# Kernel optimization log

Measured on AMD Instinct MI355X. Metric: run time of the kernel, lower is better.

Reference implementation:

```python
import jax, jax.numpy as jnp
import numpy as np

IS_CAUSAL = True


def setup_inputs() -> dict:
    key = jax.random.key(0)
    kq, kk, kv = jax.random.split(key, 3)
    q = jax.random.normal(kq, (2, 32, 2048, 128), dtype=jnp.float32)
    k = jax.random.normal(kk, (2, 8, 2048, 128), dtype=jnp.float32)
    v = jax.random.normal(kv, (2, 8, 2048, 128), dtype=jnp.float32)
    return {"q": q, "k": k, "v": v}


def reference(q, k, v):
    # q: [B, Hq, Sq, D]; k, v: [B, Hk, Sk, D] with Hq % Hk == 0 (GQA)
    B, Hq, Sq, D = q.shape
    Hk, Sk = k.shape[1], k.shape[2]
    rep = Hq // Hk
    # GQA broadcast: repeat_interleave along head dim
    k_e = jnp.repeat(k, rep, axis=1)  # [B, Hq, Sk, D]
    v_e = jnp.repeat(v, rep, axis=1)
    scale = jnp.float32(1.0 / np.sqrt(D))
    # scores in fp32 (original casts s to float32 before softmax)
    s = jnp.einsum('bhqd,bhkd->bhqk', q, k_e).astype(jnp.float32) * scale
    if IS_CAUSAL:
        mask = jnp.tril(jnp.ones((Sq, Sk), dtype=bool))  # [Sq, Sk]
        s = jnp.where(mask, s, -jnp.inf)
    p = jax.nn.softmax(s, axis=-1).astype(q.dtype)  # [B, Hq, Sq, Sk]
    attn = jnp.einsum('bhqk,bhkd->bhqd', p, v_e)
    return attn
```

## Files before the change

### kernel.cpp

```cpp
#include <hip/hip_runtime.h>


typedef __bf16 bf16_t;
typedef __bf16 bf16x2 __attribute__((ext_vector_type(2)));
typedef __bf16 bf16x8 __attribute__((ext_vector_type(8)));
typedef float f32x4v __attribute__((ext_vector_type(4)));
typedef float f32x16 __attribute__((ext_vector_type(16)));
typedef unsigned int u32;
typedef u32 u32x4 __attribute__((ext_vector_type(4)));

constexpr int B_ = 2, HQ = 32, HK = 8, SQ = 2048, D = 128;
constexpr int QT = 128, KT = 32;
constexpr int NQT = SQ / QT;
constexpr int NT = SQ / KT;
constexpr int NITEM = NQT * 64;
constexpr int NBLK = 768;
constexpr int TILE_ELEM = KT * D * 2;
constexpr size_t TILE_BYTES = TILE_ELEM * 2;
constexpr size_t WS_IMG = (size_t)B_ * HK * NT * TILE_BYTES;
constexpr size_t WS_NEED = WS_IMG + 64;

__device__ __forceinline__ u32 pkbf(float a, float b) {
  bf16x2 t; t[0] = (bf16_t)a; t[1] = (bf16_t)b;
  return __builtin_bit_cast(u32, t);
}
__device__ __forceinline__ float fexp2(float x) { return __builtin_exp2f(x); }

__device__ __forceinline__ void gl_lds16(const void* g, void* l) {
  __builtin_amdgcn_global_load_lds(
      (const __attribute__((address_space(1))) u32*)g,
      (__attribute__((address_space(3))) u32*)l, 16, 0, 0);
}

__global__ __launch_bounds__(256)
void prepass(const float* __restrict__ kg, const float* __restrict__ vg,
             bf16_t* __restrict__ ws) {
  const int blk = blockIdx.x;
  const int bh = blk >> 6, t = blk & 63;
  const float* ksrc = kg + ((size_t)bh * SQ + (size_t)t * KT) * D;
  const float* vsrc = vg + ((size_t)bh * SQ + (size_t)t * KT) * D;
  bf16_t* kdst = ws + (size_t)blk * TILE_ELEM;
  bf16_t* vdst = kdst + KT * D;
  const int tid = threadIdx.x;
#pragma unroll
  for (int i = 0; i < 2; ++i) {
    const int c = tid + 256 * i;
    const int r = c >> 4, p = c & 15, q = p ^ (r & 15);
    const float* s = ksrc + (size_t)r * D + 8 * q;
    f32x4v a = *(const f32x4v*)s;
    f32x4v b = *(const f32x4v*)(s + 4);
    bf16x8 w;
    w[0]=(bf16_t)a[0]; w[1]=(bf16_t)a[1]; w[2]=(bf16_t)a[2]; w[3]=(bf16_t)a[3];
    w[4]=(bf16_t)b[0]; w[5]=(bf16_t)b[1]; w[6]=(bf16_t)b[2]; w[7]=(bf16_t)b[3];
    *(bf16x8*)(kdst + (size_t)r * D + 8 * p) = w;
  }
#pragma unroll
  for (int i = 0; i < 2; ++i) {
    const int c = tid + 256 * i;
    const int d = c >> 2, p = c & 3, q = p ^ (d & 3);
    bf16x8 w;
#pragma unroll
    for (int j = 0; j < 8; ++j) w[j] = (bf16_t)vsrc[(size_t)(8 * q + j) * D + d];
    *(bf16x8*)(vdst + (size_t)d * KT + 8 * p) = w;
  }
}

__global__ __launch_bounds__(256, 3)
void fa6(const float* __restrict__ qg_, const bf16_t* __restrict__ ws,
         float* __restrict__ og_, int* __restrict__ cnt) {
  __shared__ __align__(16) char ldsraw[3 * TILE_BYTES];
  __shared__ int item_s;

  const int tid = threadIdx.x;
  const int wv = tid >> 6, lane = tid & 63;
  const int ln = lane & 31, hx = lane >> 5;
  const float qscale = 0.08838834764831845f * 1.4426950408889634f;

  for (;;) {
    if (tid == 0) item_s = atomicAdd(cnt, 1);
    __syncthreads();
    const int it = item_s;
    if (it >= NITEM) break;

    const int qt = (NQT - 1) - (it >> 6);
    const int bh = it & 63;
    const int b = bh >> 5, h = bh & 31, hk = h >> 2;
    const int q0 = qt * QT;
    const float* qg = qg_ + ((size_t)(b * HQ + h) * SQ + q0) * D;
    float*       og = og_ + ((size_t)(b * HQ + h) * SQ + q0) * D;
    const bf16_t* wsrc = ws + (size_t)(b * HK + hk) * NT * TILE_ELEM;
    const int ntile = q0 / KT + 4;
    const int wrow = q0 + 32 * wv;

    auto stage = [&](int tl, int buf) {
      const char* src = (const char*)(wsrc + (size_t)tl * TILE_ELEM);
      char* dst = ldsraw + (size_t)buf * TILE_BYTES;
#pragma unroll
      for (int i = 0; i < 4; ++i) {
        const int chunk = 4 * wv + i;
        gl_lds16(src + chunk * 1024 + lane * 16, dst + chunk * 1024);
      }
    };

    stage(0, 0);

    bf16x8 qf[8];
    {
      const float* qrp = qg + (size_t)(32 * wv + ln) * D + 8 * hx;
#pragma unroll
      for (int s = 0; s < 8; ++s) {
        f32x4v a = *(const f32x4v*)(qrp + 16 * s);
        f32x4v c = *(const f32x4v*)(qrp + 16 * s + 4);
        bf16x8 t;
        t[0]=(bf16_t)(a[0]*qscale); t[1]=(bf16_t)(a[1]*qscale);
        t[2]=(bf16_t)(a[2]*qscale); t[3]=(bf16_t)(a[3]*qscale);
        t[4]=(bf16_t)(c[0]*qscale); t[5]=(bf16_t)(c[1]*qscale);
        t[6]=(bf16_t)(c[2]*qscale); t[7]=(bf16_t)(c[3]*qscale);
        qf[s] = t;
      }
    }
    stage(1, 1);

    f32x16 Oa[4];
#pragma unroll
    for (int mb = 0; mb < 4; ++mb)
#pragma unroll
      for (int r = 0; r < 16; ++r) Oa[mb][r] = 0.f;
    float m = -1e30f, l = 0.f;

    int cur = 0;
    for (int t = 0; t < ntile; ++t) {
      if (t + 1 < ntile) { asm volatile("s_waitcnt vmcnt(4)" ::: "memory"); }
      else               { asm volatile("s_waitcnt vmcnt(0)" ::: "memory"); }
      __builtin_amdgcn_sched_barrier(0);
      __builtin_amdgcn_s_barrier();
      __builtin_amdgcn_sched_barrier(0);

      if (t + 2 < ntile) {
        const int sb = (cur == 0) ? 2 : cur - 1;
        stage(t + 2, sb);
      }

      const int kb = t * KT;
      if (kb <= wrow) {
        const bf16_t* kbp = (const bf16_t*)(ldsraw + (size_t)cur * TILE_BYTES);
        const bf16_t* vbp = kbp + KT * D;

        f32x16 sa;
#pragma unroll
        for (int r = 0; r < 16; ++r) sa[r] = 0.f;
        __builtin_amdgcn_s_setprio(1);
#pragma unroll
        for (int s = 0; s < 8; ++s) {
          const int cb = (2 * s + hx) ^ (ln & 15);
          bf16x8 kf = *(const bf16x8*)(kbp + ln * 128 + cb * 8);
          sa = __builtin_amdgcn_mfma_f32_32x32x16_bf16(kf, qf[s], sa, 0, 0, 0);
        }
        __builtin_amdgcn_s_setprio(0);

        if (kb == wrow) {
#pragma unroll
          for (int r = 0; r < 16; ++r) {
            const int kl = (r & 3) + 8 * (r >> 2) + 4 * hx;
            if (kl > ln) sa[r] = -1e30f;
          }
        }

        float tm = -1e30f;
#pragma unroll
        for (int r = 0; r < 16; ++r) tm = fmaxf(tm, sa[r]);
        tm = fmaxf(tm, __shfl_xor(tm, 32, 64));
        if (__any(tm > m + 8.f)) {
          const float mn = fmaxf(m, tm);
          const float corr = fexp2(m - mn);
          m = mn; l *= corr;
#pragma unroll
          for (int mb = 0; mb < 4; ++mb)
#pragma unroll
            for (int r = 0; r < 16; ++r) Oa[mb][r] *= corr;
        }
#pragma unroll
        for (int r = 0; r < 16; ++r) sa[r] = fexp2(sa[r] - m);
        float ps = 0.f;
#pragma unroll
        for (int r = 0; r < 16; ++r) ps += sa[r];
        ps += __shfl_xor(ps, 32, 64);
        l += ps;

        u32x4 pa[2];
#pragma unroll
        for (int s2 = 0; s2 < 2; ++s2) {
          const u32 A0 = pkbf(sa[8*s2+0], sa[8*s2+1]);
          const u32 A1 = pkbf(sa[8*s2+2], sa[8*s2+3]);
          const u32 B0 = pkbf(sa[8*s2+4], sa[8*s2+5]);
          const u32 B1 = pkbf(sa[8*s2+6], sa[8*s2+7]);
          const u32 r0 = __shfl_xor(hx ? A0 : B0, 32, 64);
          const u32 r1 = __shfl_xor(hx ? A1 : B1, 32, 64);
          pa[s2][0] = hx ? r0 : A0;
          pa[s2][1] = hx ? r1 : A1;
          pa[s2][2] = hx ? B0 : r0;
          pa[s2][3] = hx ? B1 : r1;
        }

        __builtin_amdgcn_s_setprio(1);
#pragma unroll
        for (int s2 = 0; s2 < 2; ++s2) {
#pragma unroll
          for (int mb = 0; mb < 4; ++mb) {
            const int d0 = ln + 32 * mb;
            const int cb = (2 * s2 + hx) ^ (d0 & 3);
            bf16x8 vf = *(const bf16x8*)(vbp + d0 * KT + cb * 8);
            Oa[mb] = __builtin_amdgcn_mfma_f32_32x32x16_bf16(
                vf, __builtin_bit_cast(bf16x8, pa[s2]), Oa[mb], 0, 0, 0);
          }
        }
        __builtin_amdgcn_s_setprio(0);
      }

      cur = (cur == 2) ? 0 : cur + 1;
    }

    asm volatile("s_waitcnt lgkmcnt(0)" ::: "memory");
    __builtin_amdgcn_s_barrier();
    __builtin_amdgcn_sched_barrier(0);

    const float inv = 1.f / l;
    float* wlds = (float*)ldsraw + wv * 2048;
#pragma unroll
    for (int h2 = 0; h2 < 2; ++h2) {
#pragma unroll
      for (int mb2 = 0; mb2 < 2; ++mb2) {
        const int mb = 2 * h2 + mb2;
#pragma unroll
        for (int g2 = 0; g2 < 4; ++g2) {
          f32x4v v4;
          v4[0] = Oa[mb][4*g2+0] * inv; v4[1] = Oa[mb][4*g2+1] * inv;
          v4[2] = Oa[mb][4*g2+2] * inv; v4[3] = Oa[mb][4*g2+3] * inv;
          const int lslot = 2 * g2 + hx + 8 * mb2;
          const int pslot = lslot ^ (ln & 15);
          *(f32x4v*)(wlds + ln * 64 + pslot * 4) = v4;
        }
      }
      asm volatile("s_waitcnt lgkmcnt(0)" ::: "memory");
      __builtin_amdgcn_sched_barrier(0);
#pragma unroll
      for (int i = 0; i < 8; ++i) {
        const int q2 = 4 * i + (lane >> 4);
        const int lsl = lane & 15;
        const int psl = lsl ^ (q2 & 15);
        f32x4v v4 = *(const f32x4v*)(wlds + q2 * 64 + psl * 4);
        *(f32x4v*)(og + (size_t)(32 * wv + q2) * D + 64 * h2 + 4 * lsl) = v4;
      }
      __builtin_amdgcn_sched_barrier(0);
    }
  }
}

namespace fb {
typedef float f32x4 __attribute__((ext_vector_type(4)));
constexpr int QT2 = 128, KT2 = 64;
constexpr int KELEM = 64 * 128, VELEM = 128 * 64, BUFE = KELEM + VELEM;

__device__ __forceinline__ u32 bfb(float f) {
  u32 u = __float_as_uint(f);
  u += 0x7fffu + ((u >> 16) & 1u);
  return u >> 16;
}
__device__ __forceinline__ bf16_t f2bf(float f) {
  unsigned short hs = (unsigned short)bfb(f);
  bf16_t b; __builtin_memcpy(&b, &hs, 2); return b;
}

__global__ __launch_bounds__(256, 2)
void fa2(const float* __restrict__ qg_, const float* __restrict__ kg_,
         const float* __restrict__ vg_, float* __restrict__ og_)
{
  __shared__ __align__(16) char ldsraw[2 * BUFE * 2];
  bf16_t* lds = (bf16_t*)ldsraw;
  const int qt = (int)gridDim.x - 1 - (int)blockIdx.x;
  const int bh = blockIdx.y;
  const int b = bh >> 5, h = bh & 31, hk = h >> 2;
  const int tid = threadIdx.x;
  const int wv = tid >> 6, lane = tid & 63;
  const int ln = lane & 31, hx = lane >> 5;
  const int q0 = qt * QT2;
  const float* qg = qg_ + ((size_t)(b * HQ + h) * SQ + q0) * D;
  const float* kg = kg_ + (size_t)(b * HK + hk) * SQ * D;
  const float* vg = vg_ + (size_t)(b * HK + hk) * SQ * D;
  float*       og = og_ + ((size_t)(b * HQ + h) * SQ + q0) * D;
  const float qscale = 0.08838834764831845f * 1.4426950408889634f;
  bf16x8 qf[8];
  {
    const float* qrow = qg + (size_t)(32 * wv + ln) * D;
#pragma unroll
    for (int s = 0; s < 8; ++s) {
      const float* p = qrow + 16 * s + 8 * hx;
      f32x4 a = *(const f32x4*)p;
      f32x4 c = *(const f32x4*)(p + 4);
      bf16x8 t;
      t[0]=f2bf(a[0]*qscale); t[1]=f2bf(a[1]*qscale);
      t[2]=f2bf(a[2]*qscale); t[3]=f2bf(a[3]*qscale);
      t[4]=f2bf(c[0]*qscale); t[5]=f2bf(c[1]*qscale);
      t[6]=f2bf(c[2]*qscale); t[7]=f2bf(c[3]*qscale);
      qf[s] = t;
    }
  }
  f32x16 Oa[4];
#pragma unroll
  for (int mb = 0; mb < 4; ++mb)
#pragma unroll
    for (int r = 0; r < 16; ++r) Oa[mb][r] = 0.f;
  float m = -1e30f, l = 0.f;
  const int qrow_g = q0 + 32 * wv + ln;
  const int wlast = q0 + 32 * wv + 31;
  const int kv_end = q0 + QT2;
  const int krow = tid >> 2, kq = tid & 3;
  const int vkh = tid & 7, vd4 = tid >> 3;
  f32x4 kst[8], vst[8];
  auto kstage_load = [&](int kb) {
    const float* src = kg + (size_t)(kb + krow) * D + kq * 32;
#pragma unroll
    for (int it = 0; it < 4; ++it) {
      kst[2*it]   = *(const f32x4*)(src + 8 * it);
      kst[2*it+1] = *(const f32x4*)(src + 8 * it + 4);
    }
  };
  auto kstage_write = [&](int buf) {
    bf16_t* kbp = lds + buf * BUFE;
#pragma unroll
    for (int it = 0; it < 4; ++it) {
      const int cb = (kq * 4 + it) ^ (krow & 7);
      bf16x8 w;
      w[0]=f2bf(kst[2*it][0]);   w[1]=f2bf(kst[2*it][1]);
      w[2]=f2bf(kst[2*it][2]);   w[3]=f2bf(kst[2*it][3]);
      w[4]=f2bf(kst[2*it+1][0]); w[5]=f2bf(kst[2*it+1][1]);
      w[6]=f2bf(kst[2*it+1][2]); w[7]=f2bf(kst[2*it+1][3]);
      *(bf16x8*)(kbp + krow * 128 + cb * 8) = w;
    }
  };
  auto vstage_load = [&](int kb) {
    const float* src = vg + (size_t)(kb + 8 * vkh) * D + 4 * vd4;
#pragma unroll
    for (int i = 0; i < 8; ++i) vst[i] = *(const f32x4*)(src + (size_t)i * D);
  };
  auto vstage_write = [&](int buf) {
    bf16_t* vbp = lds + buf * BUFE + KELEM;
#pragma unroll
    for (int j = 0; j < 4; ++j) {
      const int d = 4 * vd4 + j;
      const int cb = vkh ^ (d & 7);
      bf16x8 w;
#pragma unroll
      for (int i = 0; i < 8; ++i) w[i] = f2bf(vst[i][j]);
      *(bf16x8*)(vbp + d * 64 + cb * 8) = w;
    }
  };
  kstage_load(0); kstage_write(0);
  vstage_load(0); vstage_write(0);
  __syncthreads();
  int cur = 0;
  for (int kb = 0; kb < kv_end; kb += KT2) {
    const bool nx = (kb + KT2 < kv_end);
    const bool act = (kb <= wlast);
    if (nx) kstage_load(kb + KT2);
    u32x4 pa[4];
    if (act) {
      const bf16_t* kbp = lds + cur * BUFE;
      f32x16 s0, s1;
#pragma unroll
      for (int r = 0; r < 16; ++r) { s0[r] = 0.f; s1[r] = 0.f; }
#pragma unroll
      for (int s = 0; s < 8; ++s) {
        const int cb = (2 * s + hx) ^ (ln & 7);
        bf16x8 k0 = *(const bf16x8*)(kbp + ln * 128 + cb * 8);
        bf16x8 k1 = *(const bf16x8*)(kbp + (ln + 32) * 128 + cb * 8);
        s0 = __builtin_amdgcn_mfma_f32_32x32x16_bf16(k0, qf[s], s0, 0, 0, 0);
        s1 = __builtin_amdgcn_mfma_f32_32x32x16_bf16(k1, qf[s], s1, 0, 0, 0);
      }
      if (kb + 63 > q0 + 32 * wv) {
#pragma unroll
        for (int r = 0; r < 16; ++r) {
          const int kl = (r & 3) + 8 * (r >> 2) + 4 * hx;
          if (kb + kl > qrow_g)      s0[r] = -1e30f;
          if (kb + 32 + kl > qrow_g) s1[r] = -1e30f;
        }
      }
      float tm = -1e30f;
#pragma unroll
      for (int r = 0; r < 16; ++r) tm = fmaxf(tm, fmaxf(s0[r], s1[r]));
      tm = fmaxf(tm, __shfl_xor(tm, 32, 64));
      if (__any(tm > m + 8.f)) {
        const float mn = fmaxf(m, tm);
        const float corr = fexp2(m - mn);
        m = mn; l *= corr;
#pragma unroll
        for (int mb = 0; mb < 4; ++mb)
#pragma unroll
          for (int r = 0; r < 16; ++r) Oa[mb][r] *= corr;
      }
      f32x16 p0, p1;
#pragma unroll
      for (int r = 0; r < 16; ++r) {
        p0[r] = fexp2(s0[r] - m);
        p1[r] = fexp2(s1[r] - m);
      }
      float ps = 0.f;
#pragma unroll
      for (int r = 0; r < 16; ++r) ps += p0[r] + p1[r];
      ps += __shfl_xor(ps, 32, 64);
      l += ps;
#pragma unroll
      for (int kb2 = 0; kb2 < 2; ++kb2) {
        const f32x16& pp = kb2 ? p1 : p0;
#pragma unroll
        for (int s2 = 0; s2 < 2; ++s2) {
          const u32 A0 = pkbf(pp[8*s2+0], pp[8*s2+1]);
          const u32 A1 = pkbf(pp[8*s2+2], pp[8*s2+3]);
          const u32 B0 = pkbf(pp[8*s2+4], pp[8*s2+5]);
          const u32 B1 = pkbf(pp[8*s2+6], pp[8*s2+7]);
          const u32 sA0 = __shfl_xor(A0, 32, 64), sA1 = __shfl_xor(A1, 32, 64);
          const u32 sB0 = __shfl_xor(B0, 32, 64), sB1 = __shfl_xor(B1, 32, 64);
          const int ks = 2 * kb2 + s2;
          pa[ks][0] = hx ? sB0 : A0;
          pa[ks][1] = hx ? sB1 : A1;
          pa[ks][2] = hx ? B0 : sA0;
          pa[ks][3] = hx ? B1 : sA1;
        }
      }
    }
    if (nx) kstage_write(cur ^ 1);
    if (nx) vstage_load(kb + KT2);
    if (act) {
      const bf16_t* vbp = lds + cur * BUFE + KELEM;
#pragma unroll
      for (int mb = 0; mb < 4; ++mb) {
        const int d0 = ln + 32 * mb;
#pragma unroll
        for (int ks = 0; ks < 4; ++ks) {
          const int cb = (hx + 2 * ks) ^ (d0 & 7);
          bf16x8 vf = *(const bf16x8*)(vbp + d0 * 64 + cb * 8);
          Oa[mb] = __builtin_amdgcn_mfma_f32_32x32x16_bf16(
              vf, __builtin_bit_cast(bf16x8, pa[ks]), Oa[mb], 0, 0, 0);
        }
      }
    }
    if (nx) vstage_write(cur ^ 1);
    __syncthreads();
    cur ^= 1;
  }
  float* ol = (float*)ldsraw;
  float* wbase = ol + wv * 4096;
  const float inv = 1.f / l;
#pragma unroll
  for (int mb = 0; mb < 4; ++mb) {
#pragma unroll
    for (int g = 0; g < 4; ++g) {
      f32x4 v4;
      v4[0] = Oa[mb][4*g+0]*inv; v4[1] = Oa[mb][4*g+1]*inv;
      v4[2] = Oa[mb][4*g+2]*inv; v4[3] = Oa[mb][4*g+3]*inv;
      const int chunk = (2 * g + hx + 8 * mb) ^ (ln & 7);
      *(f32x4*)(wbase + ln * 128 + chunk * 4) = v4;
    }
  }
  __syncthreads();
#pragma unroll
  for (int i = 0; i < 16; ++i) {
    const int q2 = 2 * i + hx;
    const int cs = ln ^ (q2 & 7);
    f32x4 v4 = *(const f32x4*)(wbase + q2 * 128 + cs * 4);
    *(f32x4*)(og + (size_t)(32 * wv + q2) * D + 4 * ln) = v4;
  }
}
}

extern "C" void kernel_launch(void* const* d_in, const int* in_sizes, int n_in,
                              void* d_out, int out_size, void* d_ws, size_t ws_size,
                              hipStream_t stream) {
  const float* q = (const float*)d_in[0];
  const float* k = (const float*)d_in[1];
  const float* v = (const float*)d_in[2];
  float* out = (float*)d_out;
  if (ws_size >= WS_NEED) {
    int* cnt = (int*)((char*)d_ws + WS_IMG);
    hipMemsetAsync(cnt, 0, sizeof(int), stream);
    prepass<<<dim3(B_ * HK * NT), 256, 0, stream>>>(k, v, (bf16_t*)d_ws);
    fa6<<<dim3(NBLK), 256, 0, stream>>>(q, (const bf16_t*)d_ws, out, cnt);
  } else {
    fb::fa2<<<dim3(SQ / fb::QT2, B_ * HQ), 256, 0, stream>>>(q, k, v, out);
  }
}
```

Baseline: 147.8 us.

## Replace persistent atomic work queue with static grid and split K/V staging

Drops the persistent kernel that pulled work items through a global atomic counter and instead launches one block per (q-tile, batch-head), mapping q-tiles through a fixed permutation table to balance causal work across the grid. K and V tiles are now staged separately, with K triple-buffered and V double-buffered, and V is loaded one tile ahead instead of two. This shrinks LDS to 40 KB so four blocks can fit per CU, and removes the memset and the atomic traffic. In exchange it relies on the hardware block scheduler and the permutation to balance uneven causal work, rather than handing out the longest tiles first.

```diff
diff --git a/kernel.cpp b/kernel.cpp
--- a/kernel.cpp
+++ b/kernel.cpp
@@ -13,12 +13,10 @@
 constexpr int QT = 128, KT = 32;
 constexpr int NQT = SQ / QT;
 constexpr int NT = SQ / KT;
-constexpr int NITEM = NQT * 64;
-constexpr int NBLK = 768;
+constexpr int NBLK = NQT * 64;
 constexpr int TILE_ELEM = KT * D * 2;
 constexpr size_t TILE_BYTES = TILE_ELEM * 2;
-constexpr size_t WS_IMG = (size_t)B_ * HK * NT * TILE_BYTES;
-constexpr size_t WS_NEED = WS_IMG + 64;
+constexpr size_t WS_NEED = (size_t)B_ * HK * NT * TILE_BYTES;
 
 __device__ __forceinline__ u32 pkbf(float a, float b) {
   bf16x2 t; t[0] = (bf16_t)a; t[1] = (bf16_t)b;
@@ -65,194 +63,192 @@
   }
 }
 
-__global__ __launch_bounds__(256, 3)
-void fa6(const float* __restrict__ qg_, const bf16_t* __restrict__ ws,
-         float* __restrict__ og_, int* __restrict__ cnt) {
-  __shared__ __align__(16) char ldsraw[3 * TILE_BYTES];
-  __shared__ int item_s;
+__global__ __launch_bounds__(256, 4)
+void fa8(const float* __restrict__ qg_, const bf16_t* __restrict__ ws,
+         float* __restrict__ og_) {
+  __shared__ __align__(16) char ldsraw[40960];
+
+  constexpr int MAGIC[16] = {0,13,11,6, 14,3,5,8, 9,4,2,15, 7,10,12,1};
+  const int idx = blockIdx.x;
+  const int qt = MAGIC[(((idx >> 8) & 3) << 2) | (idx & 3)];
+  const int bh = (idx >> 2) & 63;
+  const int b = bh >> 5, h = bh & 31, hk = h >> 2;
 
   const int tid = threadIdx.x;
   const int wv = tid >> 6, lane = tid & 63;
   const int ln = lane & 31, hx = lane >> 5;
+
+  const int q0 = qt * QT;
+  const float* qg = qg_ + ((size_t)(b * HQ + h) * SQ + q0) * D;
+  float*       og = og_ + ((size_t)(b * HQ + h) * SQ + q0) * D;
+  const bf16_t* wsrc = ws + (size_t)(b * HK + hk) * NT * TILE_ELEM;
+  const int ntile = q0 / KT + 4;
+  const int wrow = q0 + 32 * wv;
+
+  auto stageK = [&](int tl) {
+    const char* src = (const char*)(wsrc + (size_t)tl * TILE_ELEM);
+    char* dst = ldsraw + (tl % 3) * 8192;
+#pragma unroll
+    for (int i = 0; i < 2; ++i) {
+      const int c = 2 * wv + i;
+      gl_lds16(src + c * 1024 + lane * 16, dst + c * 1024);
+    }
+  };
+  auto stageV = [&](int tl) {
+    const char* src = (const char*)(wsrc + (size_t)tl * TILE_ELEM) + 8192;
+    char* dst = ldsraw + 24576 + (tl & 1) * 8192;
+#pragma unroll
+    for (int i = 0; i < 2; ++i) {
+      const int c = 2 * wv + i;
+      gl_lds16(src + c * 1024 + lane * 16, dst + c * 1024);
+    }
+  };
+
   const float qscale = 0.08838834764831845f * 1.4426950408889634f;
 
-  for (;;) {
-    if (tid == 0) item_s = atomicAdd(cnt, 1);
-    __syncthreads();
-    const int it = item_s;
-    if (it >= NITEM) break;
-
-    const int qt = (NQT - 1) - (it >> 6);
-    const int bh = it & 63;
-    const int b = bh >> 5, h = bh & 31, hk = h >> 2;
-    const int q0 = qt * QT;
-    const float* qg = qg_ + ((size_t)(b * HQ + h) * SQ + q0) * D;
-    float*       og = og_ + ((size_t)(b * HQ + h) * SQ + q0) * D;
-    const bf16_t* wsrc = ws + (size_t)(b * HK + hk) * NT * TILE_ELEM;
-    const int ntile = q0 / KT + 4;
-    const int wrow = q0 + 32 * wv;
-
-    auto stage = [&](int tl, int buf) {
-      const char* src = (const char*)(wsrc + (size_t)tl * TILE_ELEM);
-      char* dst = ldsraw + (size_t)buf * TILE_BYTES;
-#pragma unroll
-      for (int i = 0; i < 4; ++i) {
-        const int chunk = 4 * wv + i;
-        gl_lds16(src + chunk * 1024 + lane * 16, dst + chunk * 1024);
-      }
-    };
-
-    stage(0, 0);
-
-    bf16x8 qf[8];
-    {
-      const float* qrp = qg + (size_t)(32 * wv + ln) * D + 8 * hx;
-#pragma unroll
-      for (int s = 0; s < 8; ++s) {
-        f32x4v a = *(const f32x4v*)(qrp + 16 * s);
-        f32x4v c = *(const f32x4v*)(qrp + 16 * s + 4);
-        bf16x8 t;
-        t[0]=(bf16_t)(a[0]*qscale); t[1]=(bf16_t)(a[1]*qscale);
-        t[2]=(bf16_t)(a[2]*qscale); t[3]=(bf16_t)(a[3]*qscale);
-        t[4]=(bf16_t)(c[0]*qscale); t[5]=(bf16_t)(c[1]*qscale);
-        t[6]=(bf16_t)(c[2]*qscale); t[7]=(bf16_t)(c[3]*qscale);
-        qf[s] = t;
-      }
-    }
-    stage(1, 1);
-
-    f32x16 Oa[4];
-#pragma unroll
-    for (int mb = 0; mb < 4; ++mb)
-#pragma unroll
-      for (int r = 0; r < 16; ++r) Oa[mb][r] = 0.f;
-    float m = -1e30f, l = 0.f;
-
-    int cur = 0;
-    for (int t = 0; t < ntile; ++t) {
-      if (t + 1 < ntile) { asm volatile("s_waitcnt vmcnt(4)" ::: "memory"); }
-      else               { asm volatile("s_waitcnt vmcnt(0)" ::: "memory"); }
-      __builtin_amdgcn_sched_barrier(0);
-      __builtin_amdgcn_s_barrier();
-      __builtin_amdgcn_sched_barrier(0);
-
-      if (t + 2 < ntile) {
-        const int sb = (cur == 0) ? 2 : cur - 1;
-        stage(t + 2, sb);
-      }
-
-      const int kb = t * KT;
-      if (kb <= wrow) {
-        const bf16_t* kbp = (const bf16_t*)(ldsraw + (size_t)cur * TILE_BYTES);
-        const bf16_t* vbp = kbp + KT * D;
-
-        f32x16 sa;
-#pragma unroll
-        for (int r = 0; r < 16; ++r) sa[r] = 0.f;
-        __builtin_amdgcn_s_setprio(1);
-#pragma unroll
-        for (int s = 0; s < 8; ++s) {
-          const int cb = (2 * s + hx) ^ (ln & 15);
-          bf16x8 kf = *(const bf16x8*)(kbp + ln * 128 + cb * 8);
-          sa = __builtin_amdgcn_mfma_f32_32x32x16_bf16(kf, qf[s], sa, 0, 0, 0);
-        }
-        __builtin_amdgcn_s_setprio(0);
-
-        if (kb == wrow) {
-#pragma unroll
-          for (int r = 0; r < 16; ++r) {
-            const int kl = (r & 3) + 8 * (r >> 2) + 4 * hx;
-            if (kl > ln) sa[r] = -1e30f;
-          }
-        }
-
-        float tm = -1e30f;
-#pragma unroll
-        for (int r = 0; r < 16; ++r) tm = fmaxf(tm, sa[r]);
-        tm = fmaxf(tm, __shfl_xor(tm, 32, 64));
-        if (__any(tm > m + 8.f)) {
-          const float mn = fmaxf(m, tm);
-          const float corr = fexp2(m - mn);
-          m = mn; l *= corr;
-#pragma unroll
-          for (int mb = 0; mb < 4; ++mb)
-#pragma unroll
-            for (int r = 0; r < 16; ++r) Oa[mb][r] *= corr;
-        }
-#pragma unroll
-        for (int r = 0; r < 16; ++r) sa[r] = fexp2(sa[r] - m);
-        float ps = 0.f;
-#pragma unroll
-        for (int r = 0; r < 16; ++r) ps += sa[r];
-        ps += __shfl_xor(ps, 32, 64);
-        l += ps;
-
-        u32x4 pa[2];
-#pragma unroll
-        for (int s2 = 0; s2 < 2; ++s2) {
-          const u32 A0 = pkbf(sa[8*s2+0], sa[8*s2+1]);
-          const u32 A1 = pkbf(sa[8*s2+2], sa[8*s2+3]);
-          const u32 B0 = pkbf(sa[8*s2+4], sa[8*s2+5]);
-          const u32 B1 = pkbf(sa[8*s2+6], sa[8*s2+7]);
-          const u32 r0 = __shfl_xor(hx ? A0 : B0, 32, 64);
-          const u32 r1 = __shfl_xor(hx ? A1 : B1, 32, 64);
-          pa[s2][0] = hx ? r0 : A0;
-          pa[s2][1] = hx ? r1 : A1;
-          pa[s2][2] = hx ? B0 : r0;
-          pa[s2][3] = hx ? B1 : r1;
-        }
-
-        __builtin_amdgcn_s_setprio(1);
-#pragma unroll
-        for (int s2 = 0; s2 < 2; ++s2) {
-#pragma unroll
-          for (int mb = 0; mb < 4; ++mb) {
-            const int d0 = ln + 32 * mb;
-            const int cb = (2 * s2 + hx) ^ (d0 & 3);
-            bf16x8 vf = *(const bf16x8*)(vbp + d0 * KT + cb * 8);
-            Oa[mb] = __builtin_amdgcn_mfma_f32_32x32x16_bf16(
-                vf, __builtin_bit_cast(bf16x8, pa[s2]), Oa[mb], 0, 0, 0);
-          }
-        }
-        __builtin_amdgcn_s_setprio(0);
-      }
-
-      cur = (cur == 2) ? 0 : cur + 1;
-    }
-
-    asm volatile("s_waitcnt lgkmcnt(0)" ::: "memory");
+  bf16x8 qf[8];
+  {
+    const float* qrp = qg + (size_t)(32 * wv + ln) * D + 8 * hx;
+#pragma unroll
+    for (int s = 0; s < 8; ++s) {
+      f32x4v a = *(const f32x4v*)(qrp + 16 * s);
+      f32x4v c = *(const f32x4v*)(qrp + 16 * s + 4);
+      bf16x8 t;
+      t[0]=(bf16_t)(a[0]*qscale); t[1]=(bf16_t)(a[1]*qscale);
+      t[2]=(bf16_t)(a[2]*qscale); t[3]=(bf16_t)(a[3]*qscale);
+      t[4]=(bf16_t)(c[0]*qscale); t[5]=(bf16_t)(c[1]*qscale);
+      t[6]=(bf16_t)(c[2]*qscale); t[7]=(bf16_t)(c[3]*qscale);
+      qf[s] = t;
+    }
+  }
+  stageK(0); stageV(0); stageK(1);
+
+  f32x16 Oa[4];
+#pragma unroll
+  for (int mb = 0; mb < 4; ++mb)
+#pragma unroll
+    for (int r = 0; r < 16; ++r) Oa[mb][r] = 0.f;
+  float m = -1e30f, l = 0.f;
+
+  for (int t = 0; t < ntile; ++t) {
+    if (t + 1 < ntile) { asm volatile("s_waitcnt vmcnt(2)" ::: "memory"); }
+    else               { asm volatile("s_waitcnt vmcnt(0)" ::: "memory"); }
+    __builtin_amdgcn_sched_barrier(0);
     __builtin_amdgcn_s_barrier();
     __builtin_amdgcn_sched_barrier(0);
 
-    const float inv = 1.f / l;
-    float* wlds = (float*)ldsraw + wv * 2048;
-#pragma unroll
-    for (int h2 = 0; h2 < 2; ++h2) {
-#pragma unroll
-      for (int mb2 = 0; mb2 < 2; ++mb2) {
-        const int mb = 2 * h2 + mb2;
-#pragma unroll
-        for (int g2 = 0; g2 < 4; ++g2) {
-          f32x4v v4;
-          v4[0] = Oa[mb][4*g2+0] * inv; v4[1] = Oa[mb][4*g2+1] * inv;
-          v4[2] = Oa[mb][4*g2+2] * inv; v4[3] = Oa[mb][4*g2+3] * inv;
-          const int lslot = 2 * g2 + hx + 8 * mb2;
-          const int pslot = lslot ^ (ln & 15);
-          *(f32x4v*)(wlds + ln * 64 + pslot * 4) = v4;
+    if (t + 1 < ntile) stageV(t + 1);
+    if (t + 2 < ntile) stageK(t + 2);
+
+    const int kb = t * KT;
+    if (kb <= wrow) {
+      const bf16_t* kbp = (const bf16_t*)(ldsraw + (t % 3) * 8192);
+      const bf16_t* vbp = (const bf16_t*)(ldsraw + 24576 + (t & 1) * 8192);
+
+      f32x16 sa;
+#pragma unroll
+      for (int r = 0; r < 16; ++r) sa[r] = 0.f;
+      __builtin_amdgcn_s_setprio(1);
+#pragma unroll
+      for (int s = 0; s < 8; ++s) {
+        const int cb = (2 * s + hx) ^ (ln & 15);
+        bf16x8 kf = *(const bf16x8*)(kbp + ln * 128 + cb * 8);
+        sa = __builtin_amdgcn_mfma_f32_32x32x16_bf16(kf, qf[s], sa, 0, 0, 0);
+      }
+      __builtin_amdgcn_s_setprio(0);
+
+      if (kb == wrow) {
+#pragma unroll
+        for (int r = 0; r < 16; ++r) {
+          const int kl = (r & 3) + 8 * (r >> 2) + 4 * hx;
+          if (kl > ln) sa[r] = -1e30f;
         }
       }
-      asm volatile("s_waitcnt lgkmcnt(0)" ::: "memory");
-      __builtin_amdgcn_sched_barrier(0);
-#pragma unroll
-      for (int i = 0; i < 8; ++i) {
-        const int q2 = 4 * i + (lane >> 4);
-        const int lsl = lane & 15;
-        const int psl = lsl ^ (q2 & 15);
-        f32x4v v4 = *(const f32x4v*)(wlds + q2 * 64 + psl * 4);
-        *(f32x4v*)(og + (size_t)(32 * wv + q2) * D + 64 * h2 + 4 * lsl) = v4;
-      }
-      __builtin_amdgcn_sched_barrier(0);
-    }
+
+      float tm = -1e30f;
+#pragma unroll
+      for (int r = 0; r < 16; ++r) tm = fmaxf(tm, sa[r]);
+      tm = fmaxf(tm, __shfl_xor(tm, 32, 64));
+      if (__any(tm > m + 8.f)) {
+        const float mn = fmaxf(m, tm);
+        const float corr = fexp2(m - mn);
+        m = mn; l *= corr;
+#pragma unroll
+        for (int mb = 0; mb < 4; ++mb)
+#pragma unroll
+          for (int r = 0; r < 16; ++r) Oa[mb][r] *= corr;
+      }
+#pragma unroll
+      for (int r = 0; r < 16; ++r) sa[r] = fexp2(sa[r] - m);
+      float ps = 0.f;
+#pragma unroll
+      for (int r = 0; r < 16; ++r) ps += sa[r];
+      ps += __shfl_xor(ps, 32, 64);
+      l += ps;
+
+      u32x4 pa[2];
+#pragma unroll
+      for (int s2 = 0; s2 < 2; ++s2) {
+        const u32 A0 = pkbf(sa[8*s2+0], sa[8*s2+1]);
+        const u32 A1 = pkbf(sa[8*s2+2], sa[8*s2+3]);
+        const u32 B0 = pkbf(sa[8*s2+4], sa[8*s2+5]);
+        const u32 B1 = pkbf(sa[8*s2+6], sa[8*s2+7]);
+        const u32 r0 = __shfl_xor(hx ? A0 : B0, 32, 64);
+        const u32 r1 = __shfl_xor(hx ? A1 : B1, 32, 64);
+        pa[s2][0] = hx ? r0 : A0;
+        pa[s2][1] = hx ? r1 : A1;
+        pa[s2][2] = hx ? B0 : r0;
+        pa[s2][3] = hx ? B1 : r1;
+      }
+
+      __builtin_amdgcn_s_setprio(1);
+#pragma unroll
+      for (int s2 = 0; s2 < 2; ++s2) {
+#pragma unroll
+        for (int mb = 0; mb < 4; ++mb) {
+          const int d0 = ln + 32 * mb;
+          const int cb = (2 * s2 + hx) ^ (d0 & 3);
+          bf16x8 vf = *(const bf16x8*)(vbp + d0 * KT + cb * 8);
+          Oa[mb] = __builtin_amdgcn_mfma_f32_32x32x16_bf16(
+              vf, __builtin_bit_cast(bf16x8, pa[s2]), Oa[mb], 0, 0, 0);
+        }
+      }
+      __builtin_amdgcn_s_setprio(0);
+    }
+  }
+
+  asm volatile("s_waitcnt lgkmcnt(0)" ::: "memory");
+  __builtin_amdgcn_s_barrier();
+  __builtin_amdgcn_sched_barrier(0);
+
+  const float inv = 1.f / l;
+  float* wlds = (float*)ldsraw + wv * 2048;
+#pragma unroll
+  for (int h2 = 0; h2 < 2; ++h2) {
+#pragma unroll
+    for (int mb2 = 0; mb2 < 2; ++mb2) {
+      const int mb = 2 * h2 + mb2;
+#pragma unroll
+      for (int g2 = 0; g2 < 4; ++g2) {
+        f32x4v v4;
+        v4[0] = Oa[mb][4*g2+0] * inv; v4[1] = Oa[mb][4*g2+1] * inv;
+        v4[2] = Oa[mb][4*g2+2] * inv; v4[3] = Oa[mb][4*g2+3] * inv;
+        const int lslot = 2 * g2 + hx + 8 * mb2;
+        const int pslot = lslot ^ (ln & 15);
+        *(f32x4v*)(wlds + ln * 64 + pslot * 4) = v4;
+      }
+    }
+    asm volatile("s_waitcnt lgkmcnt(0)" ::: "memory");
+    __builtin_amdgcn_sched_barrier(0);
+#pragma unroll
+    for (int i = 0; i < 8; ++i) {
+      const int q2 = 4 * i + (lane >> 4);
+      const int lsl = lane & 15;
+      const int psl = lsl ^ (q2 & 15);
+      f32x4v v4 = *(const f32x4v*)(wlds + q2 * 64 + psl * 4);
+      *(f32x4v*)(og + (size_t)(32 * wv + q2) * D + 64 * h2 + 4 * lsl) = v4;
+    }
+    __builtin_amdgcn_sched_barrier(0);
   }
 }
 
@@ -481,10 +477,8 @@
   const float* v = (const float*)d_in[2];
   float* out = (float*)d_out;
   if (ws_size >= WS_NEED) {
-    int* cnt = (int*)((char*)d_ws + WS_IMG);
-    hipMemsetAsync(cnt, 0, sizeof(int), stream);
     prepass<<<dim3(B_ * HK * NT), 256, 0, stream>>>(k, v, (bf16_t*)d_ws);
-    fa6<<<dim3(NBLK), 256, 0, stream>>>(q, (const bf16_t*)d_ws, out, cnt);
+    fa8<<<dim3(NBLK), 256, 0, stream>>>(q, (const bf16_t*)d_ws, out);
   } else {
     fb::fa2<<<dim3(SQ / fb::QT2, B_ * HQ), 256, 0, stream>>>(q, k, v, out);
   }
```

Measured after the change: 229.0 us. +54.9%, slower.
